# Optimization experiments

Hardware: AMD Instinct MI355X
Metric: run time of the kernel (lower is better)

The kernel has to match this reference:

```python
import jax, jax.numpy as jnp
import numpy as np
import itertools

# ---- model dimensions ----
NELEC = 10   # total electrons
NSPIN = 2    # spin_split = 2 -> equal split (5, 5)
NPER = 5     # electrons per spin block
D = 3        # spatial dimension
NION = 2     # number of ions (diatomic)
DP = 32      # backflow output feature dim d'
NDENSE = 64  # ndense_resnet


def _perms_and_signs(n):
    perms = np.array(list(itertools.permutations(range(n))), dtype=np.int32)
    signs = np.empty(len(perms), dtype=np.float32)
    for i, p in enumerate(perms):
        inv = sum(1 for a in range(n) for b in range(a + 1, n) if p[a] > p[b])
        signs[i] = -1.0 if inv % 2 else 1.0
    return jnp.asarray(perms), jnp.asarray(signs)

# constant permutation indices/signs (closed over; not differentiated)
PERMS, SIGNS = _perms_and_signs(NPER)  # (120, 5), (120,)


def setup_inputs() -> dict:
    key = jax.random.key(0)
    ks = jax.random.split(key, 8)
    B = 2048
    feat = NION * D + NION  # backflow input features per electron: r_ei flat + |r_ei|
    nin = NPER * DP         # flattened spin-block input to each ResNet
    return {
        "elec_pos": jax.random.normal(ks[0], (B, NELEC, D), jnp.float32),
        "ion_pos": jax.random.normal(ks[1], (NION, D), jnp.float32) * 2.0,
        "bf_w": jax.random.normal(ks[2], (feat, DP), jnp.float32) / np.sqrt(feat),
        "bf_b": jnp.zeros((DP,), jnp.float32),
        "w0": jax.random.normal(ks[3], (NSPIN, nin, NDENSE), jnp.float32) / np.sqrt(nin),
        "b0": jnp.zeros((NSPIN, NDENSE), jnp.float32),
        "w1": jax.random.normal(ks[4], (NSPIN, NDENSE, NDENSE), jnp.float32) / np.sqrt(NDENSE),
        "b1": jnp.zeros((NSPIN, NDENSE), jnp.float32),
        "w2": jax.random.normal(ks[5], (NSPIN, NDENSE, 1), jnp.float32) / np.sqrt(NDENSE),
        "b2": jnp.zeros((NSPIN, 1), jnp.float32),
        "jastrow_kernel": jnp.ones((NION,), jnp.float32),
    }


def _spin_antisym(block, W0, B0, W1, B1, W2, B2):
    # block: (B, NPER, DP) one spin block of the 1e stream
    B = block.shape[0]
    xp = block[:, PERMS, :]                  # (B, nperm, NPER, DP) all permutations
    xp = xp.reshape(B, PERMS.shape[0], NPER * DP)
    # SimpleResNet: dense->act, residual middle layer, final linear to 1
    h = jnp.tanh(xp @ W0 + B0)
    h = jnp.tanh(h @ W1 + B1) + h            # residual (shapes match)
    out = (h @ W2 + B2)[..., 0]              # (B, nperm)
    return jnp.sum(out * SIGNS, axis=-1)     # signed perm-sum -> (B,)


def reference(elec_pos, ion_pos, bf_w, bf_b, w0, b0, w1, b1, w2, b2, jastrow_kernel):
    B = elec_pos.shape[0]
    # backflow: r_ei features -> dense -> tanh
    r_ei = elec_pos[..., :, None, :] - ion_pos          # (B, nelec, nion, d)
    r_norm = jnp.linalg.norm(r_ei, axis=-1)             # (B, nelec, nion)
    feats = jnp.concatenate([r_ei.reshape(B, NELEC, NION * D), r_norm], axis=-1)
    stream_1e = jnp.tanh(feats @ bf_w + bf_b)           # (B, nelec, DP)
    # split into equal spin blocks (spin_split=2)
    blocks = jnp.stack(jnp.split(stream_1e, NSPIN, axis=-2), axis=0)  # (NSPIN, B, NPER, DP)
    per_spin = jax.vmap(_spin_antisym)(blocks, w0, b0, w1, b1, w2, b2)  # (NSPIN, B)
    antisymmetric_part = jnp.log(jnp.abs(jnp.prod(per_spin, axis=0)))   # (B,)
    # isotropic atomic exponential decay jastrow (log domain)
    jastrow_part = -jnp.sum(jastrow_kernel * r_norm, axis=(-1, -2))     # (B,)
    return antisymmetric_part + jastrow_part
```

## Files before the change

### kernel.cpp

```cpp
#include <hip/hip_runtime.h>
#include <math.h>

#define NELEC 10
#define NSPIN 2
#define NPER 5
#define DIM 3
#define NION 2
#define DP 32
#define NDENSE 64
#define NPERM 120
#define RS 324
#define SAW 1780
#define HT2S 248
#define HTK 32

#define POOL_WORDS (HTK * HT2S)

typedef float v2f __attribute__((ext_vector_type(2)));
typedef float v4f __attribute__((ext_vector_type(4)));

#define PK_FMA_LO(acc, hp, wp) \
    asm("v_pk_fma_f32 %0, %1, %2, %0 op_sel_hi:[1,0,1]" : "+v"(acc) : "v"(hp), "v"(wp))
#define PK_FMA_HI(acc, hp, wp) \
    asm("v_pk_fma_f32 %0, %1, %2, %0 op_sel:[0,1,0] op_sel_hi:[1,1,1]" : "+v"(acc) : "v"(hp), "v"(wp))

__device__ __forceinline__ float fast_tanh(float x) {
    float e = __expf(2.0f * x);
    return 1.0f - 2.0f * __builtin_amdgcn_rcpf(e + 1.0f);
}

__device__ __forceinline__ unsigned pick_remove(unsigned& el, int d) {
    unsigned v = (el >> (4 * d)) & 0xFu;
    unsigned low = el & ((1u << (4 * d)) - 1u);
    el = low | ((el >> (4 * (d + 1))) << (4 * d));
    return v;
}

__global__ __launch_bounds__(256, 1) void antisym_fused(
    const float* __restrict__ elec_pos, const float* __restrict__ ion_pos,
    const float* __restrict__ bf_w, const float* __restrict__ bf_b,
    const float* __restrict__ w0, const float* __restrict__ b0,
    const float* __restrict__ w1, const float* __restrict__ b1,
    const float* __restrict__ w2, const float* __restrict__ jk,
    float* __restrict__ out, int B)
{
    const int b = blockIdx.x;
    const int t = threadIdx.x;
    const int s = t >> 7;
    const int ts = t & 127;
    const int wave = (t >> 6) & 1;
    const int lane = t & 63;

    __shared__ __align__(16) float pool[POOL_WORDS];
    __shared__ double red_h[NSPIN][2];
    __shared__ double red_j[NSPIN][2];
    __shared__ float jterm[2 * NELEC];

    float* s1e = pool + s * SAW;
    #define GROW(j) (pool + s * SAW + 160 + (j) * RS)
    #define HT32(k) (pool + (k) * HT2S)

    const float* ep = elec_pos + (b * NELEC + s * NPER) * DIM;
    const float i0x = ion_pos[0], i0y = ion_pos[1], i0z = ion_pos[2];
    const float i1x = ion_pos[3], i1y = ion_pos[4], i1z = ion_pos[5];
    for (int idx = ts; idx < NPER * DP; idx += 128) {
        int j = idx >> 5, c = idx & 31;
        float ex = ep[j * 3 + 0], ey = ep[j * 3 + 1], ez = ep[j * 3 + 2];
        float dx0 = ex - i0x, dy0 = ey - i0y, dz0 = ez - i0z;
        float dx1 = ex - i1x, dy1 = ey - i1y, dz1 = ez - i1z;
        float n0 = sqrtf(dx0 * dx0 + dy0 * dy0 + dz0 * dz0);
        float n1 = sqrtf(dx1 * dx1 + dy1 * dy1 + dz1 * dz1);
        float acc = bf_b[c];
        acc += dx0 * bf_w[0 * DP + c];
        acc += dy0 * bf_w[1 * DP + c];
        acc += dz0 * bf_w[2 * DP + c];
        acc += dx1 * bf_w[3 * DP + c];
        acc += dy1 * bf_w[4 * DP + c];
        acc += dz1 * bf_w[5 * DP + c];
        acc += n0 * bf_w[6 * DP + c];
        acc += n1 * bf_w[7 * DP + c];
        s1e[idx] = fast_tanh(acc);
    }
    if (t < 2 * NELEC) {
        int e = t >> 1, ion = t & 1;
        const float* epb = elec_pos + b * NELEC * DIM;
        float ex = epb[e * 3 + 0], ey = epb[e * 3 + 1], ez = epb[e * 3 + 2];
        float ix = ion_pos[ion * 3 + 0], iy = ion_pos[ion * 3 + 1], iz = ion_pos[ion * 3 + 2];
        float dx = ex - ix, dy = ey - iy, dz = ez - iz;
        jterm[t] = jk[ion] * sqrtf(dx * dx + dy * dy + dz * dz);
    }
    __syncthreads();

    const float* w0s = w0 + s * (NPER * DP) * NDENSE;
    for (int j = wave; j < NPER; j += 2) {
        float4 sv4[8];
        #pragma unroll
        for (int q = 0; q < 8; q++) sv4[q] = *(const float4*)(s1e + j * DP + q * 4);
        #pragma unroll
        for (int i = 0; i < NPER; i++) {
            float acc = 0.f;
            #pragma unroll
            for (int q = 0; q < 8; q++) {
                const float* wb = w0s + (i * DP + q * 4) * NDENSE + lane;
                acc += sv4[q].x * wb[0 * NDENSE];
                acc += sv4[q].y * wb[1 * NDENSE];
                acc += sv4[q].z * wb[2 * NDENSE];
                acc += sv4[q].w * wb[3 * NDENSE];
            }
            GROW(j)[i * NDENSE + lane] = acc;
        }
    }
    __syncthreads();

    const float* b0s = b0 + s * NDENSE;
    const float* w2s = w2 + s * NDENSE;

    const int pid = wave * 60 + lane;
    float sign = 0.f;
    int p0 = 0, p1 = 0, p2 = 0, p3 = 0, p4 = 0;
    if (lane < 60) {
        int p = pid;
        unsigned el = 0x43210u;
        int d0 = p / 24; p -= d0 * 24;
        int d1 = p / 6;  p -= d1 * 6;
        int d2 = p / 2;  p -= d2 * 2;
        int d3 = p;
        p0 = pick_remove(el, d0);
        p1 = pick_remove(el, d1);
        p2 = pick_remove(el, d2);
        p3 = pick_remove(el, d3);
        p4 = el & 0xF;
        sign = ((d0 + d1 + d2 + d3) & 1) ? -1.f : 1.f;
    }
    const float* g0 = GROW(p0) + 0 * NDENSE;
    const float* g1 = GROW(p1) + 1 * NDENSE;
    const float* g2 = GROW(p2) + 2 * NDENSE;
    const float* g3 = GROW(p3) + 3 * NDENSE;
    const float* g4 = GROW(p4) + 4 * NDENSE;

    float h[NDENSE];
    float hdot = 0.f;
    #pragma unroll
    for (int cc = 0; cc < NDENSE / 4; cc++) {
        float4 a = *(const float4*)(b0s + cc * 4);
        float4 q;
        q = *(const float4*)(g0 + cc * 4); a.x += q.x; a.y += q.y; a.z += q.z; a.w += q.w;
        q = *(const float4*)(g1 + cc * 4); a.x += q.x; a.y += q.y; a.z += q.z; a.w += q.w;
        q = *(const float4*)(g2 + cc * 4); a.x += q.x; a.y += q.y; a.z += q.z; a.w += q.w;
        q = *(const float4*)(g3 + cc * 4); a.x += q.x; a.y += q.y; a.z += q.z; a.w += q.w;
        q = *(const float4*)(g4 + cc * 4); a.x += q.x; a.y += q.y; a.z += q.z; a.w += q.w;
        float t0 = fast_tanh(a.x), t1 = fast_tanh(a.y), t2 = fast_tanh(a.z), t3 = fast_tanh(a.w);
        h[cc * 4 + 0] = t0; h[cc * 4 + 1] = t1; h[cc * 4 + 2] = t2; h[cc * 4 + 3] = t3;
        hdot += t0 * w2s[cc * 4 + 0] + t1 * w2s[cc * 4 + 1]
              + t2 * w2s[cc * 4 + 2] + t3 * w2s[cc * 4 + 3];
    }

    double dvh = (double)(sign * hdot);
    #pragma unroll
    for (int off = 32; off > 0; off >>= 1) dvh += __shfl_down(dvh, off, 64);
    if (lane == 0) red_h[s][wave] = dvh;

    __syncthreads();

    const int pg = lane >> 3, jg = lane & 7;
    const int pbl = wave ? (56 + 8 * pg) : (8 * pg);
    const int pb = pbl + 124 * s;
    const float* w1s = w1 + s * NDENSE * NDENSE;
    const float* b1s = b1 + s * NDENSE;
    const float* wgp = w1s + 8 * jg;

    v2f vp[4][8];
    #pragma unroll
    for (int ip = 0; ip < 4; ip++)
        #pragma unroll
        for (int r = 0; r < 8; r++) vp[ip][r] = (v2f)(0.f);

    #pragma unroll 1
    for (int half = 0; half < 2; half++) {
        if (lane < 60) {
            #pragma unroll
            for (int kk = 0; kk < HTK; kk++)
                HT32(kk)[124 * s + pid] = h[half * HTK + kk];
        }
        __syncthreads();

        const float* wh = wgp + half * HTK * NDENSE;
        v4f ha_n = *(const v4f*)(&HT32(0)[pb]);
        v4f hb_n = *(const v4f*)(&HT32(0)[pb + 4]);
        v4f wa_n = *(const v4f*)(wh);
        v4f wb_n = *(const v4f*)(wh + 4);
        #pragma unroll 4
        for (int kk = 0; kk < HTK; kk++) {
            const v4f ha = ha_n, hb = hb_n, wa = wa_n, wb = wb_n;
            if (kk + 1 < HTK) {
                ha_n = *(const v4f*)(&HT32(kk + 1)[pb]);
                hb_n = *(const v4f*)(&HT32(kk + 1)[pb + 4]);
                wa_n = *(const v4f*)(wh + (kk + 1) * NDENSE);
                wb_n = *(const v4f*)(wh + (kk + 1) * NDENSE + 4);
            }
            v2f hp[4] = {ha.xy, ha.zw, hb.xy, hb.zw};
            v2f wp[4] = {wa.xy, wa.zw, wb.xy, wb.zw};
            #pragma unroll
            for (int ip = 0; ip < 4; ip++) {
                PK_FMA_LO(vp[ip][0], hp[ip], wp[0]);
                PK_FMA_HI(vp[ip][1], hp[ip], wp[0]);
                PK_FMA_LO(vp[ip][2], hp[ip], wp[1]);
                PK_FMA_HI(vp[ip][3], hp[ip], wp[1]);
                PK_FMA_LO(vp[ip][4], hp[ip], wp[2]);
                PK_FMA_HI(vp[ip][5], hp[ip], wp[2]);
                PK_FMA_LO(vp[ip][6], hp[ip], wp[3]);
                PK_FMA_HI(vp[ip][7], hp[ip], wp[3]);
            }
        }
        if (half == 0) __syncthreads();
    }

    float4 b1a = *(const float4*)(b1s + 8 * jg);
    float4 b1b = *(const float4*)(b1s + 8 * jg + 4);
    float4 w2a = *(const float4*)(w2s + 8 * jg);
    float4 w2b = *(const float4*)(w2s + 8 * jg + 4);
    const float b1v[8] = {b1a.x, b1a.y, b1a.z, b1a.w, b1b.x, b1b.y, b1b.z, b1b.w};
    const float w2v[8] = {w2a.x, w2a.y, w2a.z, w2a.w, w2b.x, w2b.y, w2b.z, w2b.w};

    float lanesum = 0.f;
    #pragma unroll
    for (int i = 0; i < 8; i++) {
        int p = pbl + i;
        int d0 = p / 24;  int r0 = p - 24 * d0;
        int d1 = r0 / 6;  int r1 = r0 - 6 * d1;
        int d2 = r1 >> 1; int d3 = r1 & 1;
        float sgn = ((d0 + d1 + d2 + d3) & 1) ? -1.f : 1.f;
        if (wave == 1 && pg == 0) sgn = 0.f;
        float si = 0.f;
        #pragma unroll
        for (int r = 0; r < 8; r++) {
            float vir = (i & 1) ? vp[i >> 1][r].y : vp[i >> 1][r].x;
            si = fmaf(fast_tanh(vir + b1v[r]), w2v[r], si);
        }
        lanesum = fmaf(sgn, si, lanesum);
    }

    double dvj = (double)lanesum;
    #pragma unroll
    for (int off = 32; off > 0; off >>= 1) dvj += __shfl_down(dvj, off, 64);
    if (lane == 0) red_j[s][wave] = dvj;
    __syncthreads();

    if (t == 0) {
        float ps0 = (float)((red_h[0][0] + red_h[0][1]) + (red_j[0][0] + red_j[0][1]));
        float ps1 = (float)((red_h[1][0] + red_h[1][1]) + (red_j[1][0] + red_j[1][1]));
        float jas = 0.f;
        #pragma unroll
        for (int i = 0; i < 2 * NELEC; i++) jas += jterm[i];
        out[b] = logf(fabsf(ps0 * ps1)) - jas;
    }
}

extern "C" void kernel_launch(void* const* d_in, const int* in_sizes, int n_in,
                              void* d_out, int out_size, void* d_ws, size_t ws_size,
                              hipStream_t stream) {
    const float* elec_pos = (const float*)d_in[0];
    const float* ion_pos  = (const float*)d_in[1];
    const float* bf_w     = (const float*)d_in[2];
    const float* bf_b     = (const float*)d_in[3];
    const float* w0       = (const float*)d_in[4];
    const float* b0       = (const float*)d_in[5];
    const float* w1       = (const float*)d_in[6];
    const float* b1       = (const float*)d_in[7];
    const float* w2       = (const float*)d_in[8];
    const float* jk       = (const float*)d_in[10];
    float* out = (float*)d_out;

    const int B = in_sizes[0] / (NELEC * DIM);

    hipLaunchKernelGGL(antisym_fused,
                       dim3(B), dim3(256), 0, stream,
                       elec_pos, ion_pos, bf_w, bf_b, w0, b0, w1, b1, w2, jk, out, B);
}
```

Measured before the change: 182.7 us.

## Compute first-layer activations per half to cut register pressure

Each half's 32 first-layer tanh activations are now computed just before they are staged into shared memory, instead of holding all 64 in registers across a barrier. The hidden-product scratch area gets its own region of the shared pool so it no longer overlaps the per-spin backflow and G rows, which removes one barrier. The aim is fewer live registers and possibly higher occupancy. The cost is a larger shared-memory pool and a fully unrolled half loop, which grows code size.

```diff
diff --git a/kernel.cpp b/kernel.cpp
--- a/kernel.cpp
+++ b/kernel.cpp
@@ -10,11 +10,11 @@
 #define NDENSE 64
 #define NPERM 120
 #define RS 324
-#define SAW 1780
 #define HT2S 248
 #define HTK 32
-
-#define POOL_WORDS (HTK * HT2S)
+#define HTBASE 3560
+#define POOL_WORDS (HTBASE + HTK * HT2S)
+
 
 typedef float v2f __attribute__((ext_vector_type(2)));
 typedef float v4f __attribute__((ext_vector_type(4)));
@@ -56,9 +56,9 @@
     __shared__ double red_j[NSPIN][2];
     __shared__ float jterm[2 * NELEC];
 
-    float* s1e = pool + s * SAW;
-    #define GROW(j) (pool + s * SAW + 160 + (j) * RS)
-    #define HT32(k) (pool + (k) * HT2S)
+    float* s1e = pool + s * 160;
+    #define GROW(j) (pool + 320 + s * (NPER * RS) + (j) * RS)
+    #define HT32(k) (pool + HTBASE + (k) * HT2S)
 
     const float* ep = elec_pos + (b * NELEC + s * NPER) * DIM;
     const float i0x = ion_pos[0], i0y = ion_pos[1], i0z = ion_pos[2];
@@ -138,30 +138,6 @@
     const float* g3 = GROW(p3) + 3 * NDENSE;
     const float* g4 = GROW(p4) + 4 * NDENSE;
 
-    float h[NDENSE];
-    float hdot = 0.f;
-    #pragma unroll
-    for (int cc = 0; cc < NDENSE / 4; cc++) {
-        float4 a = *(const float4*)(b0s + cc * 4);
-        float4 q;
-        q = *(const float4*)(g0 + cc * 4); a.x += q.x; a.y += q.y; a.z += q.z; a.w += q.w;
-        q = *(const float4*)(g1 + cc * 4); a.x += q.x; a.y += q.y; a.z += q.z; a.w += q.w;
-        q = *(const float4*)(g2 + cc * 4); a.x += q.x; a.y += q.y; a.z += q.z; a.w += q.w;
-        q = *(const float4*)(g3 + cc * 4); a.x += q.x; a.y += q.y; a.z += q.z; a.w += q.w;
-        q = *(const float4*)(g4 + cc * 4); a.x += q.x; a.y += q.y; a.z += q.z; a.w += q.w;
-        float t0 = fast_tanh(a.x), t1 = fast_tanh(a.y), t2 = fast_tanh(a.z), t3 = fast_tanh(a.w);
-        h[cc * 4 + 0] = t0; h[cc * 4 + 1] = t1; h[cc * 4 + 2] = t2; h[cc * 4 + 3] = t3;
-        hdot += t0 * w2s[cc * 4 + 0] + t1 * w2s[cc * 4 + 1]
-              + t2 * w2s[cc * 4 + 2] + t3 * w2s[cc * 4 + 3];
-    }
-
-    double dvh = (double)(sign * hdot);
-    #pragma unroll
-    for (int off = 32; off > 0; off >>= 1) dvh += __shfl_down(dvh, off, 64);
-    if (lane == 0) red_h[s][wave] = dvh;
-
-    __syncthreads();
-
     const int pg = lane >> 3, jg = lane & 7;
     const int pbl = wave ? (56 + 8 * pg) : (8 * pg);
     const int pb = pbl + 124 * s;
@@ -169,18 +145,34 @@
     const float* b1s = b1 + s * NDENSE;
     const float* wgp = w1s + 8 * jg;
 
+    float hdot = 0.f;
     v2f vp[4][8];
     #pragma unroll
     for (int ip = 0; ip < 4; ip++)
         #pragma unroll
         for (int r = 0; r < 8; r++) vp[ip][r] = (v2f)(0.f);
 
-    #pragma unroll 1
+    #pragma unroll
     for (int half = 0; half < 2; half++) {
+        float hh[HTK];
+        #pragma unroll
+        for (int cc = 0; cc < 8; cc++) {
+            const int c4 = half * HTK + cc * 4;
+            float4 a = *(const float4*)(b0s + c4);
+            float4 q;
+            q = *(const float4*)(g0 + c4); a.x += q.x; a.y += q.y; a.z += q.z; a.w += q.w;
+            q = *(const float4*)(g1 + c4); a.x += q.x; a.y += q.y; a.z += q.z; a.w += q.w;
+            q = *(const float4*)(g2 + c4); a.x += q.x; a.y += q.y; a.z += q.z; a.w += q.w;
+            q = *(const float4*)(g3 + c4); a.x += q.x; a.y += q.y; a.z += q.z; a.w += q.w;
+            q = *(const float4*)(g4 + c4); a.x += q.x; a.y += q.y; a.z += q.z; a.w += q.w;
+            float t0 = fast_tanh(a.x), t1 = fast_tanh(a.y), t2 = fast_tanh(a.z), t3 = fast_tanh(a.w);
+            hh[cc * 4 + 0] = t0; hh[cc * 4 + 1] = t1; hh[cc * 4 + 2] = t2; hh[cc * 4 + 3] = t3;
+            hdot += t0 * w2s[c4 + 0] + t1 * w2s[c4 + 1]
+                  + t2 * w2s[c4 + 2] + t3 * w2s[c4 + 3];
+        }
         if (lane < 60) {
             #pragma unroll
-            for (int kk = 0; kk < HTK; kk++)
-                HT32(kk)[124 * s + pid] = h[half * HTK + kk];
+            for (int kk = 0; kk < HTK; kk++) HT32(kk)[124 * s + pid] = hh[kk];
         }
         __syncthreads();
 
@@ -215,6 +207,11 @@
         if (half == 0) __syncthreads();
     }
 
+    double dvh = (double)(sign * hdot);
+    #pragma unroll
+    for (int off = 32; off > 0; off >>= 1) dvh += __shfl_down(dvh, off, 64);
+    if (lane == 0) red_h[s][wave] = dvh;
+
     float4 b1a = *(const float4*)(b1s + 8 * jg);
     float4 b1b = *(const float4*)(b1s + 8 * jg + 4);
     float4 w2a = *(const float4*)(w2s + 8 * jg);
```

After: 158.9 us. 13.0% less time.
